# Kernel tuning notes

Measured on AMD Instinct MI355X. Metric: run time of the kernel, lower is better.

The kernel has to match this reference:

```python
import jax, jax.numpy as jnp
import numpy as np

CHANS = [32, 32, 64, 64, 128, 128]
IN_CHANS = [1, 32, 32, 64, 64, 128]
BETA = 0.25  # VectorQuantizer_reset default; ResidualVQ's beta=0.4 is never forwarded
BN_EPS = 1e-5


def setup_inputs() -> dict:
    key = jax.random.key(0)
    ks = jax.random.split(key, 20)
    B, L, IDIM, H, NE = 64, 2000, 80, 256, 1024
    inp = {"speech": jax.random.normal(ks[0], (B, L, IDIM), jnp.float32)}
    for i, (ci, co) in enumerate(zip(IN_CHANS, CHANS)):
        inp[f"cw{i}"] = jax.random.normal(ks[1 + i], (co, ci, 3, 3), jnp.float32) * 0.05
        inp[f"g{i}"] = jnp.ones((co,), jnp.float32)
        inp[f"b{i}"] = jnp.zeros((co,), jnp.float32)
    inp["w_ih"] = jax.random.normal(ks[10], (3 * H, 256), jnp.float32) * 0.05
    inp["w_hh"] = jax.random.normal(ks[11], (3 * H, H), jnp.float32) * 0.05
    inp["bih"] = jnp.zeros((3 * H,), jnp.float32)
    inp["bhh"] = jnp.zeros((3 * H,), jnp.float32)
    for j, k in zip((1, 2, 3), (12, 13, 14)):
        inp[f"cb{j}"] = jax.random.uniform(ks[k], (NE, H), jnp.float32, -1.0 / NE, 1.0 / NE)
    return inp


def conv_bn_relu(x, w, g, b):
    # Conv2d(k=3, stride=2, pad=1, bias=False) + BatchNorm2d (training-mode batch stats) + ReLU
    y = jax.lax.conv_general_dilated(x, w, (2, 2), [(1, 1), (1, 1)],
                                     dimension_numbers=("NCHW", "OIHW", "NCHW"))
    mu = jnp.mean(y, axis=(0, 2, 3), keepdims=True)
    var = jnp.mean((y - mu) ** 2, axis=(0, 2, 3), keepdims=True)  # biased, as torch BN
    y = (y - mu) * jax.lax.rsqrt(var + BN_EPS) * g.reshape(1, -1, 1, 1) + b.reshape(1, -1, 1, 1)
    return jax.nn.relu(y)


def gru_last_hidden(x, w_ih, w_hh, bih, bhh):
    # x: (B, T, D). PyTorch GRU, 1 layer, h0 = 0; returns last hidden state (B, H).
    B = x.shape[0]
    H = w_hh.shape[1]
    xw = jnp.einsum("btd,gd->btg", x, w_ih) + bih  # (B, T, 3H), precompute input gates

    def step(h, xt):
        gh = h @ w_hh.T + bhh
        i_r, i_z, i_n = jnp.split(xt, 3, axis=-1)
        h_r, h_z, h_n = jnp.split(gh, 3, axis=-1)
        r = jax.nn.sigmoid(i_r + h_r)
        z = jax.nn.sigmoid(i_z + h_z)
        n = jnp.tanh(i_n + r * h_n)
        return (1.0 - z) * n + z * h, None

    h0 = jnp.zeros((B, H), x.dtype)
    hT, _ = jax.lax.scan(step, h0, jnp.swapaxes(xw, 0, 1))
    return hT


def vq(z, E):
    # z: (B, e_dim), E: (n_e, e_dim). Nearest-neighbor quantize + straight-through.
    d = jnp.sum(z * z, axis=1, keepdims=True) + jnp.sum(E * E, axis=1) - 2.0 * (z @ E.T)
    idx = jnp.argmin(d, axis=1)  # (B,)
    z_q = E[idx]
    loss = jnp.mean((jax.lax.stop_gradient(z_q) - z) ** 2) \
         + BETA * jnp.mean((z_q - jax.lax.stop_gradient(z)) ** 2)
    z_q_st = z + jax.lax.stop_gradient(z_q - z)
    return z_q_st, loss, idx


def reference(speech, cw0, g0, b0, cw1, g1, b1, cw2, g2, b2, cw3, g3, b3,
              cw4, g4, b4, cw5, g5, b5, w_ih, w_hh, bih, bhh, cb1, cb2, cb3):
    x = speech[:, None, :, :]  # (B, 1, L, idim)
    for w, g, b in ((cw0, g0, b0), (cw1, g1, b1), (cw2, g2, b2),
                    (cw3, g3, b3), (cw4, g4, b4), (cw5, g5, b5)):
        x = conv_bn_relu(x, w, g, b)
    B, C, T, F = x.shape
    hs = x.transpose(0, 2, 1, 3).reshape(B, T, C * F)  # (B, T', C*F)
    ref_embs = gru_last_hidden(hs, w_ih, w_hh, bih, bhh)  # (B, 256)

    residual = ref_embs
    zq1, l1, i1 = vq(residual, cb1)
    residual = residual - zq1
    zq2, l2, i2 = vq(residual, cb2)
    residual = residual - zq2
    zq3, l3, i3 = vq(residual, cb3)

    z_q_out = jnp.concatenate([zq1, zq2, zq3], axis=1)  # (B, 3*e_dim)
    vq_loss = l1 + l2 + l3
    codebooks = (zq1, zq2, zq3, zq1 + zq2 + zq3)
    return (z_q_out, vq_loss, i1[:, None], codebooks)
```

## Files before the change

kernel.cpp:

```cpp
#include <hip/hip_runtime.h>
#include <math.h>


__global__ __launch_bounds__(256) void prep_kernel(
    const float* __restrict__ w_ih, const float* __restrict__ w_hh,
    const float* __restrict__ cb0, const float* __restrict__ cb1,
    const float* __restrict__ cb2, float* __restrict__ w_ihT,
    float* __restrict__ w_hhT, float* __restrict__ ET, float* __restrict__ sE) {
  int tid = threadIdx.x;
  int y = blockIdx.y;
  if (y < 5) {
    const float* in;
    float* outp;
    int R, C;
    if (y == 0) { in = w_ih; outp = w_ihT; R = 768; C = 256; }
    else if (y == 1) { in = w_hh; outp = w_hhT; R = 768; C = 256; }
    else {
      in = (y == 2 ? cb0 : (y == 3 ? cb1 : cb2));
      outp = ET + (size_t)(y - 2) * 262144;
      R = 1024; C = 256;
    }
    int n = R * C;
    for (int t = blockIdx.x * 256 + tid; t < n; t += 64 * 256) {
      int i = t / C, j = t % C;
      outp[(size_t)j * R + i] = in[t];
    }
  } else {
    int wid = tid >> 6, lane = tid & 63;
    for (int c = blockIdx.x * 4 + wid; c < 3072; c += 64 * 4) {
      const float* E = (c < 1024 ? cb0 : (c < 2048 ? cb1 : cb2));
      int cc = c & 1023;
      float4 v4 = ((const float4*)(E + (size_t)cc * 256))[lane];
      float ssum = v4.x * v4.x + v4.y * v4.y + v4.z * v4.z + v4.w * v4.w;
#pragma unroll
      for (int m = 32; m >= 1; m >>= 1) ssum += __shfl_xor(ssum, m, 64);
      if (lane == 0) sE[c] = ssum;
    }
  }
}

__global__ __launch_bounds__(256) void conv0_stats_kernel(
    const float* __restrict__ speech, const float* __restrict__ w0,
    float* __restrict__ part) {
  constexpr int SPR = 41, SPH = 49;
  __shared__ float spE[SPH * SPR];
  __shared__ float spO[SPH * SPR];
  const int tid = threadIdx.x;
  const int bx = blockIdx.x;
  const int b = blockIdx.z;
  const int to0 = bx * 24;
  const int sr0 = 2 * to0 - 1;
  const float* sb = speech + (size_t)b * 160000;
  for (int i = tid; i < SPH * 81; i += 256) {
    int r = i / 81, c = i % 81;
    int gr = sr0 + r, gc = c - 1;
    float v = (gr >= 0 && gr < 2000 && gc >= 0 && gc < 80) ? sb[gr * 80 + gc] : 0.f;
    float* pl = (c & 1) ? spO : spE;
    pl[r * SPR + (c >> 1)] = v;
  }
  __syncthreads();

  const int fo = tid % 40;
  const int trr = tid / 40;
  const bool rowok = (trr < 6);
  const int r0 = rowok ? trr * 4 : 0;

  float xv4[4][9];
  {
    int e0 = (2 * r0) * SPR + fo;
    float p0 = spE[e0], p1 = spO[e0], p2 = spE[e0 + 1];
#pragma unroll
    for (int k = 0; k < 4; ++k) {
      int mr = (2 * (r0 + k) + 1) * SPR + fo;
      int br = mr + SPR;
      xv4[k][0] = p0; xv4[k][1] = p1; xv4[k][2] = p2;
      xv4[k][3] = spE[mr]; xv4[k][4] = spO[mr]; xv4[k][5] = spE[mr + 1];
      xv4[k][6] = spE[br]; xv4[k][7] = spO[br]; xv4[k][8] = spE[br + 1];
      p0 = xv4[k][6]; p1 = xv4[k][7]; p2 = xv4[k][8];
    }
  }
  bool val[4];
#pragma unroll
  for (int k = 0; k < 4; ++k) val[k] = rowok && (to0 + r0 + k < 1000);

  float s[32], q[32];
#pragma unroll
  for (int c = 0; c < 32; ++c) { s[c] = 0.f; q[c] = 0.f; }
#pragma unroll
  for (int c = 0; c < 32; ++c) {
    const float* wk = w0 + c * 9;
    float w0v = wk[0], w1v = wk[1], w2v = wk[2], w3v = wk[3], w4v = wk[4];
    float w5v = wk[5], w6v = wk[6], w7v = wk[7], w8v = wk[8];
#pragma unroll
    for (int k = 0; k < 4; ++k) {
      float a = xv4[k][0] * w0v;
      a = fmaf(xv4[k][1], w1v, a); a = fmaf(xv4[k][2], w2v, a);
      a = fmaf(xv4[k][3], w3v, a); a = fmaf(xv4[k][4], w4v, a);
      a = fmaf(xv4[k][5], w5v, a); a = fmaf(xv4[k][6], w6v, a);
      a = fmaf(xv4[k][7], w7v, a); a = fmaf(xv4[k][8], w8v, a);
      if (val[k]) { s[c] += a; q[c] = fmaf(a, a, q[c]); }
    }
  }
  const int wid = tid >> 6;
  const int lane = tid & 63;
  const int pidx = ((b * 42 + bx) << 2) | wid;
#pragma unroll
  for (int c = 0; c < 32; ++c) {
    float ss = s[c], qq = q[c];
#pragma unroll
    for (int m = 32; m >= 1; m >>= 1) {
      ss += __shfl_xor(ss, m, 64);
      qq += __shfl_xor(qq, m, 64);
    }
    if (lane == 0) {
      part[(size_t)c * 10752 + pidx] = ss;
      part[(size_t)(32 + c) * 10752 + pidx] = qq;
    }
  }
}

__global__ __launch_bounds__(256) void conv1_fused_kernel(
    const float* __restrict__ speech, const float* __restrict__ w0,
    const float* __restrict__ aff0, const float* __restrict__ w1,
    float* __restrict__ y) {
  constexpr int SPR = 41, SPH = 51;
  constexpr int LPS = 21, LTH = 25, LPL = LTH * LPS;
  __shared__ float spE[SPH * SPR];
  __shared__ float spO[SPH * SPR];
  __shared__ float l0t[2][2 * LPL];
  const int tid = threadIdx.x;
  const int bx = blockIdx.x;
  const int b = blockIdx.z;
  const int to0 = bx * 12;
  const int l0r0 = 2 * to0 - 1;
  const int sr0 = 4 * to0 - 3;
  const float* sb = speech + (size_t)b * 160000;
  for (int i = tid; i < SPH * 81; i += 256) {
    int r = i / 81, c = i % 81;
    int gr = sr0 + r, gc = c - 1;
    float v = (gr >= 0 && gr < 2000 && gc >= 0 && gc < 80) ? sb[gr * 80 + gc] : 0.f;
    float* pl = (c & 1) ? spO : spE;
    pl[r * SPR + (c >> 1)] = v;
  }

  const int fc = tid % 42;
  const int fr0 = tid / 42;
  const bool filler = (tid < 210);
  const int wcol = fc - 1;
  const bool colok = (wcol >= 0) && (wcol < 40);
  const int wc = colok ? wcol : 0;
  const int r0 = fr0 * 5;
  const int lplane = (fc & 1) * LPL;
  const int lidx = fc >> 1;

  const int fo = tid % 20;
  const int tr = tid / 20;
  const int to = to0 + tr;
  const bool active = (tr < 12) && (to < 500);
  const int trc = (tr < 12) ? tr : 0;

  float acc[32];
#pragma unroll
  for (int c = 0; c < 32; ++c) acc[c] = 0.f;

  __syncthreads();

#define L0FILL(CIDX, BF)                                                      \
  if (filler) {                                                               \
    const float* wk = w0 + (CIDX) * 9;                                        \
    const float wv0 = wk[0], wv1 = wk[1], wv2 = wk[2], wv3 = wk[3];           \
    const float wv4 = wk[4], wv5 = wk[5], wv6 = wk[6], wv7 = wk[7];           \
    const float wv8 = wk[8];                                                  \
    const float sc = aff0[CIDX], sh = aff0[32 + (CIDX)];                      \
    int e0 = (2 * r0) * SPR + wc;                                             \
    float t0 = spE[e0], t1 = spO[e0], t2 = spE[e0 + 1];                       \
    _Pragma("unroll")                                                         \
    for (int k = 0; k < 5; ++k) {                                             \
      int r = r0 + k;                                                         \
      int mr = (2 * r + 1) * SPR + wc;                                        \
      int br = mr + SPR;                                                      \
      float m0 = spE[mr], m1 = spO[mr], m2 = spE[mr + 1];                     \
      float b0 = spE[br], b1 = spO[br], b2 = spE[br + 1];                     \
      float a = t0 * wv0;                                                     \
      a = fmaf(t1, wv1, a); a = fmaf(t2, wv2, a);                             \
      a = fmaf(m0, wv3, a); a = fmaf(m1, wv4, a); a = fmaf(m2, wv5, a);       \
      a = fmaf(b0, wv6, a); a = fmaf(b1, wv7, a); a = fmaf(b2, wv8, a);       \
      int h0 = l0r0 + r;                                                      \
      bool ok = colok && h0 >= 0 && h0 < 1000;                                \
      float vv = ok ? fmaxf(fmaf(a, sc, sh), 0.f) : 0.f;                      \
      l0t[BF][lplane + r * LPS + lidx] = vv;                                  \
      t0 = b0; t1 = b1; t2 = b2;                                              \
    }                                                                         \
  }

  L0FILL(0, 0)
  __syncthreads();

  for (int ci = 0; ci < 32; ++ci) {
    int cur = ci & 1;
    if (ci + 1 < 32) { L0FILL(ci + 1, cur ^ 1) }
    float xv[9];
    const int rb = 2 * trc;
#pragma unroll
    for (int t = 0; t < 9; ++t) {
      int dr = t / 3, m = t % 3;
      xv[t] = l0t[cur][(m == 1 ? LPL : 0) + (rb + dr) * LPS + fo + (m == 2 ? 1 : 0)];
    }
    const float* wp = w1 + ci * 9;
#pragma unroll
    for (int c = 0; c < 32; ++c) {
      const float* wcp = wp + (size_t)c * 32 * 9;
#pragma unroll
      for (int t = 0; t < 9; ++t) acc[c] = fmaf(xv[t], wcp[t], acc[c]);
    }
    __syncthreads();
  }
#undef L0FILL

  if (active) {
#pragma unroll
    for (int c = 0; c < 32; ++c)
      y[(((size_t)b * 32 + c) * 500 + to) * 20 + fo] = acc[c];
  }
}

template <int CI, int COG, int WO, int ROWS, int WI, int HI, int HO>
__global__ __launch_bounds__(256) void conv_kernel(
    const float* __restrict__ x, const float* __restrict__ w,
    const float* __restrict__ aff, float* __restrict__ y, int CO) {
  constexpr int TW = WI + 2;
  constexpr int PE = (TW + 1) / 2;
  constexpr int PS = PE | 1;
  constexpr int TH = 2 * ROWS + 1;
  constexpr int PL = TH * PS;
  constexpr int TN = TH * TW;
  constexpr int F = (TN + 255) / 256;
  __shared__ float tile[2][2 * PL];

  const int tid = threadIdx.x;
  const int fo = tid % WO;
  const int tr = tid / WO;
  const int to0 = blockIdx.x * ROWS;
  const int to = to0 + tr;
  const int co0 = blockIdx.y * COG;
  const int b = blockIdx.z;
  const bool active = (tr < ROWS) && (to < HO);
  const int trc = (tr < ROWS) ? tr : 0;

  int fa[F], fof[F];
  bool fv[F], fw[F];
#pragma unroll
  for (int j = 0; j < F; ++j) {
    int i = tid + j * 256;
    int r = i / TW, c = i % TW;
    int gih = 2 * to0 - 1 + r;
    int giw = c - 1;
    bool inb = (i < TN);
    bool v = inb && gih >= 0 && gih < HI && giw >= 0 && giw < WI;
    fw[j] = inb;
    fv[j] = v;
    fof[j] = v ? (gih * WI + giw) : 0;
    fa[j] = inb ? ((c & 1) * PL + r * PS + (c >> 1)) : 0;
  }

  float acc[COG];
#pragma unroll
  for (int c = 0; c < COG; ++c) acc[c] = 0.f;

  const float* xb = x + (size_t)b * CI * HI * WI;

  {
    const float sc = aff[0], sh = aff[CI];
#pragma unroll
    for (int j = 0; j < F; ++j) {
      if (fw[j]) {
        float v = xb[fof[j]];
        v = fv[j] ? fmaxf(fmaf(v, sc, sh), 0.f) : 0.f;
        tile[0][fa[j]] = v;
      }
    }
  }
  __syncthreads();

  for (int ci = 0; ci < CI; ++ci) {
    int cur = ci & 1;
    if (ci + 1 < CI) {
      const float* xc = xb + (size_t)(ci + 1) * HI * WI;
      const float sc = aff[ci + 1], sh = aff[CI + ci + 1];
#pragma unroll
      for (int j = 0; j < F; ++j) {
        if (fw[j]) {
          float v = xc[fof[j]];
          v = fv[j] ? fmaxf(fmaf(v, sc, sh), 0.f) : 0.f;
          tile[cur ^ 1][fa[j]] = v;
        }
      }
    }
    float xv[9];
    const int rb = 2 * trc;
#pragma unroll
    for (int t = 0; t < 9; ++t) {
      int dr = t / 3, m = t % 3;
      xv[t] = tile[cur][(m == 1 ? PL : 0) + (rb + dr) * PS + fo + (m == 2 ? 1 : 0)];
    }
    const float* wp = w + ((size_t)co0 * CI + ci) * 9;
#pragma unroll
    for (int c = 0; c < COG; ++c) {
      const float* wc = wp + (size_t)c * CI * 9;
#pragma unroll
      for (int t = 0; t < 9; ++t) acc[c] = fmaf(xv[t], wc[t], acc[c]);
    }
    __syncthreads();
  }

  if (active) {
#pragma unroll
    for (int c = 0; c < COG; ++c)
      y[(((size_t)b * CO + co0 + c) * HO + to) * WO + fo] = acc[c];
  }
}

__global__ __launch_bounds__(256) void conv5_kernel(
    const float* __restrict__ x, const float* __restrict__ w5,
    const float* __restrict__ aff, float* __restrict__ part5) {
  constexpr int TW = 5, PS = 3, TH = 65, PL = TH * PS, TN = TH * TW;
  __shared__ float tile[2][2 * PL];
  const int tid = threadIdx.x;
  const int p = tid & 63;
  const int to = p >> 1, fo = p & 1;
  const int cog = tid >> 6;
  const int co0 = cog * 32;
  const int ci0 = blockIdx.y * 32;
  const int b = blockIdx.z;

  int fa[2], fof[2];
  bool fv[2], fw[2];
#pragma unroll
  for (int j = 0; j < 2; ++j) {
    int i = tid + j * 256;
    int r = i / TW, c = i % TW;
    int gih = r - 1, giw = c - 1;
    bool inb = (i < TN);
    bool v = inb && gih >= 0 && gih < 63 && giw >= 0 && giw < 3;
    fw[j] = inb;
    fv[j] = v;
    fof[j] = v ? (gih * 3 + giw) : 0;
    fa[j] = inb ? ((c & 1) * PL + r * PS + (c >> 1)) : 0;
  }

  float acc[32];
#pragma unroll
  for (int c = 0; c < 32; ++c) acc[c] = 0.f;

  const float* xb = x + (size_t)b * 128 * 189;

  {
    const float sc = aff[ci0], sh = aff[128 + ci0];
    const float* xc = xb + (size_t)ci0 * 189;
#pragma unroll
    for (int j = 0; j < 2; ++j) {
      if (fw[j]) {
        float v = xc[fof[j]];
        v = fv[j] ? fmaxf(fmaf(v, sc, sh), 0.f) : 0.f;
        tile[0][fa[j]] = v;
      }
    }
  }
  __syncthreads();

  for (int cc = 0; cc < 32; ++cc) {
    int cur = cc & 1;
    int ci = ci0 + cc;
    if (cc + 1 < 32) {
      const float* xc = xb + (size_t)(ci + 1) * 189;
      const float sc = aff[ci + 1], sh = aff[128 + ci + 1];
#pragma unroll
      for (int j = 0; j < 2; ++j) {
        if (fw[j]) {
          float v = xc[fof[j]];
          v = fv[j] ? fmaxf(fmaf(v, sc, sh), 0.f) : 0.f;
          tile[cur ^ 1][fa[j]] = v;
        }
      }
    }
    float xv[9];
#pragma unroll
    for (int t = 0; t < 9; ++t) {
      int dr = t / 3, m = t % 3;
      xv[t] = tile[cur][(m == 1 ? PL : 0) + (2 * to + dr) * PS + fo + (m == 2 ? 1 : 0)];
    }
    const float* wp = w5 + ((size_t)co0 * 128 + ci) * 9;
#pragma unroll
    for (int c = 0; c < 32; ++c) {
      const float* wc = wp + (size_t)c * 128 * 9;
#pragma unroll
      for (int t = 0; t < 9; ++t) acc[c] = fmaf(xv[t], wc[t], acc[c]);
    }
    __syncthreads();
  }

#pragma unroll
  for (int c = 0; c < 32; ++c)
    part5[(((size_t)blockIdx.y * 64 + b) * 128 + co0 + c) * 64 + p] = acc[c];
}

__global__ __launch_bounds__(256) void reduce4_kernel(const float* __restrict__ p,
                                                      float* __restrict__ y) {
  int i = blockIdx.x * 256 + threadIdx.x;
  if (i < 524288)
    y[i] = p[i] + p[i + 524288] + p[i + 2 * 524288] + p[i + 3 * 524288];
}

__global__ __launch_bounds__(256) void stats_kernel(const float* __restrict__ x,
                                                    float* __restrict__ part,
                                                    int C, int HW) {
  int c = blockIdx.x, b = blockIdx.y, tid = threadIdx.x;
  const float* xb = x + ((size_t)b * C + c) * HW;
  float s = 0.f, q = 0.f;
  for (int i = tid; i < HW; i += 256) {
    float v = xb[i];
    s += v;
    q = fmaf(v, v, q);
  }
#pragma unroll
  for (int m = 32; m >= 1; m >>= 1) {
    s += __shfl_xor(s, m, 64);
    q += __shfl_xor(q, m, 64);
  }
  if ((tid & 63) == 0) {
    int w = tid >> 6;
    part[(size_t)c * 256 + b * 4 + w] = s;
    part[(size_t)(C + c) * 256 + b * 4 + w] = q;
  }
}

__global__ __launch_bounds__(256) void bn_finalize(
    const float* __restrict__ part, const float* __restrict__ g,
    const float* __restrict__ bb, float* __restrict__ aff, int CO, int P,
    double invN) {
  __shared__ double s1[256];
  __shared__ double s2[256];
  int c = blockIdx.x, tid = threadIdx.x;
  double a = 0, q = 0;
  for (int i = tid; i < P; i += 256) {
    a += (double)part[(size_t)c * P + i];
    q += (double)part[(size_t)(CO + c) * P + i];
  }
  s1[tid] = a;
  s2[tid] = q;
  __syncthreads();
  for (int s = 128; s > 0; s >>= 1) {
    if (tid < s) { s1[tid] += s1[tid + s]; s2[tid] += s2[tid + s]; }
    __syncthreads();
  }
  if (tid == 0) {
    double mean = s1[0] * invN;
    double var = s2[0] * invN - mean * mean;
    float scale = g[c] * (float)(1.0 / sqrt(var + 1e-5));
    aff[c] = scale;
    aff[CO + c] = bb[c] - (float)mean * scale;
  }
}

__global__ __launch_bounds__(256) void xw_kernel(const float* __restrict__ act5,
                                                 const float* __restrict__ aff5,
                                                 const float* __restrict__ w_ihT,
                                                 const float* __restrict__ bih,
                                                 float* __restrict__ xw) {
  __shared__ float sh[8 * 256];
  int tid = threadIdx.x;
  int bt0 = blockIdx.x * 8;
  int b = bt0 >> 5;
  for (int i = tid; i < 2048; i += 256) {
    int r = i >> 8, d = i & 255, c = d >> 1, f = d & 1;
    int t = (bt0 + r) & 31;
    float v = act5[(((size_t)b * 128 + c) * 32 + t) * 2 + f];
    sh[i] = fmaxf(fmaf(v, aff5[c], aff5[128 + c]), 0.f);
  }
  __syncthreads();
  float acc[3][8];
#pragma unroll
  for (int g = 0; g < 3; ++g)
#pragma unroll
    for (int r = 0; r < 8; ++r) acc[g][r] = 0.f;
  for (int k = 0; k < 256; ++k) {
    float w0 = w_ihT[k * 768 + tid];
    float w1 = w_ihT[k * 768 + 256 + tid];
    float w2 = w_ihT[k * 768 + 512 + tid];
#pragma unroll
    for (int r = 0; r < 8; ++r) {
      float hv = sh[r * 256 + k];
      acc[0][r] = fmaf(hv, w0, acc[0][r]);
      acc[1][r] = fmaf(hv, w1, acc[1][r]);
      acc[2][r] = fmaf(hv, w2, acc[2][r]);
    }
  }
  float b0 = bih[tid], b1 = bih[256 + tid], b2 = bih[512 + tid];
  for (int r = 0; r < 8; ++r) {
    size_t base = (size_t)(bt0 + r) * 768;
    xw[base + tid] = acc[0][r] + b0;
    xw[base + 256 + tid] = acc[1][r] + b1;
    xw[base + 512 + tid] = acc[2][r] + b2;
  }
}

__global__ __launch_bounds__(768) void gru_kernel(const float* __restrict__ xw,
                                                  const float* __restrict__ w_hhT,
                                                  const float* __restrict__ bhh,
                                                  float* __restrict__ zout) {
  __shared__ __align__(16) float h[256];
  __shared__ float gh[768];
  int b = blockIdx.x, j = threadIdx.x;
  if (j < 256) h[j] = 0.f;
  __syncthreads();
  float bh = bhh[j];
  for (int t = 0; t < 32; ++t) {
    float acc = 0.f;
    const float4* h4 = (const float4*)h;
#pragma unroll 8
    for (int k4 = 0; k4 < 64; ++k4) {
      float4 hv = h4[k4];
      const float* wr = w_hhT + (4 * k4) * 768 + j;
      acc = fmaf(hv.x, wr[0], acc);
      acc = fmaf(hv.y, wr[768], acc);
      acc = fmaf(hv.z, wr[1536], acc);
      acc = fmaf(hv.w, wr[2304], acc);
    }
    gh[j] = acc + bh;
    __syncthreads();
    if (j < 256) {
      const float* xt = xw + ((size_t)b * 32 + t) * 768;
      float ir = xt[j], iz = xt[256 + j], inn = xt[512 + j];
      float r = 1.f / (1.f + expf(-(ir + gh[j])));
      float zz = 1.f / (1.f + expf(-(iz + gh[256 + j])));
      float n = tanhf(fmaf(r, gh[512 + j], inn));
      h[j] = (1.f - zz) * n + zz * h[j];
    }
    __syncthreads();
  }
  if (j < 256) zout[(size_t)b * 256 + j] = h[j];
}

__global__ __launch_bounds__(256) void vq_all_kernel(
    const float* __restrict__ zb, const float* __restrict__ ET,
    const float* __restrict__ sE, const float* __restrict__ cb0,
    const float* __restrict__ cb1, const float* __restrict__ cb2,
    float* __restrict__ out, float* __restrict__ msep) {
  const size_t OFF_I1 = 49153;
  const size_t OFF_CB = 49217;
  const size_t OFF_CBSUM = 98369;
  __shared__ float rz[256];
  __shared__ float rs[256];
  __shared__ int ri[256];
  int b = blockIdx.x, tid = threadIdx.x;
  float z0 = zb[(size_t)b * 256 + tid];
  rz[tid] = z0;
  float zqs = 0.f;
  for (int s = 0; s < 3; ++s) {
    __syncthreads();
    const float* ETs = ET + (size_t)s * 262144;
    const float* sEs = sE + s * 1024;
    const float* E = (s == 0 ? cb0 : (s == 1 ? cb1 : cb2));
    float a0 = 0.f, a1 = 0.f, a2 = 0.f, a3 = 0.f;
    for (int k = 0; k < 256; ++k) {
      float zk = rz[k];
      const float* row = ETs + (size_t)k * 1024 + tid;
      a0 = fmaf(zk, row[0], a0);
      a1 = fmaf(zk, row[256], a1);
      a2 = fmaf(zk, row[512], a2);
      a3 = fmaf(zk, row[768], a3);
    }
    float s0 = sEs[tid] - 2.f * a0;
    float s1 = sEs[256 + tid] - 2.f * a1;
    float s2 = sEs[512 + tid] - 2.f * a2;
    float s3 = sEs[768 + tid] - 2.f * a3;
    float bs = s0;
    int bi = tid;
    if (s1 < bs) { bs = s1; bi = 256 + tid; }
    if (s2 < bs) { bs = s2; bi = 512 + tid; }
    if (s3 < bs) { bs = s3; bi = 768 + tid; }
    rs[tid] = bs;
    ri[tid] = bi;
    __syncthreads();
    for (int st = 128; st > 0; st >>= 1) {
      if (tid < st) {
        float os = rs[tid + st];
        int oi = ri[tid + st];
        if (os < rs[tid] || (os == rs[tid] && oi < ri[tid])) {
          rs[tid] = os;
          ri[tid] = oi;
        }
      }
      __syncthreads();
    }
    int idx = ri[0];
    if (s == 0 && tid == 0) out[OFF_I1 + b] = (float)idx;
    float zq = E[(size_t)idx * 256 + tid];
    float rv = rz[tid];
    float d = zq - rv;
    out[(size_t)b * 768 + s * 256 + tid] = zq;
    out[OFF_CB + (size_t)s * 16384 + (size_t)b * 256 + tid] = zq;
    zqs += zq;
    rz[tid] = rv - zq;
    rs[tid] = d * d;
    __syncthreads();
    for (int st = 128; st > 0; st >>= 1) {
      if (tid < st) rs[tid] += rs[tid + st];
      __syncthreads();
    }
    if (tid == 0) msep[s * 64 + b] = rs[0];
  }
  out[OFF_CBSUM + (size_t)b * 256 + tid] = zqs;
}

__global__ void loss_kernel(const float* __restrict__ msep, float* __restrict__ out) {
  if (threadIdx.x == 0 && blockIdx.x == 0) {
    float s = 0.f;
    for (int i = 0; i < 192; ++i) s += msep[i];
    out[0] = 1.25f * s / 16384.0f;
  }
}

extern "C" void kernel_launch(void* const* d_in, const int* in_sizes, int n_in,
                              void* d_out, int out_size, void* d_ws, size_t ws_size,
                              hipStream_t stream) {
  const float* speech = (const float*)d_in[0];
  const float* cw[6];
  const float* gg[6];
  const float* bbp[6];
  for (int i = 0; i < 6; ++i) {
    cw[i] = (const float*)d_in[1 + 3 * i];
    gg[i] = (const float*)d_in[2 + 3 * i];
    bbp[i] = (const float*)d_in[3 + 3 * i];
  }
  const float* w_ih = (const float*)d_in[19];
  const float* w_hh = (const float*)d_in[20];
  const float* bih = (const float*)d_in[21];
  const float* bhh = (const float*)d_in[22];
  const float* cb[3] = {(const float*)d_in[23], (const float*)d_in[24], (const float*)d_in[25]};
  float* out = (float*)d_out;
  float* ws_f = (float*)d_ws;
  (void)in_sizes; (void)n_in; (void)out_size;

  size_t off = 0;
  float* act1 = ws_f + off; off += 20480000ull;
  float* act2 = ws_f + off; off += 10240000ull;
  float* act3 = ws_f + off; off += 2560000ull;
  float* part = ws_f + off; off += 700000ull;
  float* affs = ws_f + off; off += 1536ull;
  float* w_ihT = ws_f + off; off += 196608ull;
  float* w_hhT = ws_f + off; off += 196608ull;
  float* xw = ws_f + off; off += 1572864ull;
  float* zb = ws_f + off; off += 16384ull;
  float* ET = ws_f + off; off += 786432ull;
  float* sEp = ws_f + off; off += 3072ull;
  float* msep = ws_f + off; off += 192ull;

  if (ws_size < off * sizeof(float)) return;

  float* part5 = act1;
  float* act4 = act2;
  float* act5 = act3;

  const size_t OFF_LOSS = 49152;

  prep_kernel<<<dim3(64, 6), 256, 0, stream>>>(w_ih, w_hh, cb[0], cb[1], cb[2],
                                               w_ihT, w_hhT, ET, sEp);

  conv0_stats_kernel<<<dim3(42, 1, 64), 256, 0, stream>>>(speech, cw[0], part);
  bn_finalize<<<32, 256, 0, stream>>>(part, gg[0], bbp[0], affs + 0, 32, 10752,
                                      1.0 / 2560000.0);
  conv1_fused_kernel<<<dim3(42, 1, 64), 256, 0, stream>>>(speech, cw[0], affs + 0,
                                                          cw[1], act1);
  stats_kernel<<<dim3(32, 64), 256, 0, stream>>>(act1, part, 32, 10000);
  bn_finalize<<<32, 256, 0, stream>>>(part, gg[1], bbp[1], affs + 256, 32, 256,
                                      1.0 / 640000.0);
  conv_kernel<32, 32, 10, 25, 20, 500, 250>
      <<<dim3(10, 2, 64), 256, 0, stream>>>(act1, cw[2], affs + 256, act2, 64);
  stats_kernel<<<dim3(64, 64), 256, 0, stream>>>(act2, part, 64, 2500);
  bn_finalize<<<64, 256, 0, stream>>>(part, gg[2], bbp[2], affs + 512, 64, 256,
                                      1.0 / 160000.0);
  conv_kernel<64, 16, 5, 42, 10, 250, 125>
      <<<dim3(3, 4, 64), 256, 0, stream>>>(act2, cw[3], affs + 512, act3, 64);
  stats_kernel<<<dim3(64, 64), 256, 0, stream>>>(act3, part, 64, 625);
  bn_finalize<<<64, 256, 0, stream>>>(part, gg[3], bbp[3], affs + 768, 64, 256,
                                      1.0 / 40000.0);
  conv_kernel<64, 16, 3, 63, 5, 125, 63>
      <<<dim3(1, 8, 64), 256, 0, stream>>>(act3, cw[4], affs + 768, act4, 128);
  stats_kernel<<<dim3(128, 64), 256, 0, stream>>>(act4, part, 128, 189);
  bn_finalize<<<128, 256, 0, stream>>>(part, gg[4], bbp[4], affs + 1024, 128, 256,
                                       1.0 / 12096.0);
  conv5_kernel<<<dim3(1, 4, 64), 256, 0, stream>>>(act4, cw[5], affs + 1024, part5);
  reduce4_kernel<<<2048, 256, 0, stream>>>(part5, act5);
  stats_kernel<<<dim3(128, 64), 256, 0, stream>>>(act5, part, 128, 64);
  bn_finalize<<<128, 256, 0, stream>>>(part, gg[5], bbp[5], affs + 1280, 128, 256,
                                       1.0 / 4096.0);

  xw_kernel<<<256, 256, 0, stream>>>(act5, affs + 1280, w_ihT, bih, xw);
  gru_kernel<<<64, 768, 0, stream>>>(xw, w_hhT, bhh, zb);

  vq_all_kernel<<<64, 256, 0, stream>>>(zb, ET, sEp, cb[0], cb[1], cb[2], out, msep);
  loss_kernel<<<1, 64, 0, stream>>>(msep, out + OFF_LOSS);
}
```

Baseline: 1.182 ms.

## Recompute layer-0 conv in registers inside conv1, drop shared staging and barriers

Replaces the conv1 kernel that staged BN-ReLU'd layer-0 outputs per input channel in double-buffered shared memory with a kernel where each thread loads a 7x7 input patch into registers and recomputes its 3x3 layer-0 neighbourhood per channel. This removes per-channel __syncthreads and shared traffic, and uses a 240-thread block so all threads produce outputs. A pre-transposed copy of the conv1 weights is produced in the prep kernel for contiguous per-channel access. The cost is redundant layer-0 FMAs across neighbouring threads and higher register pressure.

After: 1.210 ms. 2.3% more time.

```diff
diff --git a/kernel.cpp b/kernel.cpp
--- a/kernel.cpp
+++ b/kernel.cpp
@@ -5,8 +5,9 @@
 __global__ __launch_bounds__(256) void prep_kernel(
     const float* __restrict__ w_ih, const float* __restrict__ w_hh,
     const float* __restrict__ cb0, const float* __restrict__ cb1,
-    const float* __restrict__ cb2, float* __restrict__ w_ihT,
-    float* __restrict__ w_hhT, float* __restrict__ ET, float* __restrict__ sE) {
+    const float* __restrict__ cb2, const float* __restrict__ cw1,
+    float* __restrict__ w_ihT, float* __restrict__ w_hhT,
+    float* __restrict__ ET, float* __restrict__ sE, float* __restrict__ w1T) {
   int tid = threadIdx.x;
   int y = blockIdx.y;
   if (y < 5) {
@@ -25,7 +26,7 @@
       int i = t / C, j = t % C;
       outp[(size_t)j * R + i] = in[t];
     }
-  } else {
+  } else if (y == 5) {
     int wid = tid >> 6, lane = tid & 63;
     for (int c = blockIdx.x * 4 + wid; c < 3072; c += 64 * 4) {
       const float* E = (c < 1024 ? cb0 : (c < 2048 ? cb1 : cb2));
@@ -35,6 +36,14 @@
 #pragma unroll
       for (int m = 32; m >= 1; m >>= 1) ssum += __shfl_xor(ssum, m, 64);
       if (lane == 0) sE[c] = ssum;
+    }
+  } else {
+    for (int t = blockIdx.x * 256 + tid; t < 9216; t += 64 * 256) {
+      int q = t % 9;
+      int rc = t / 9;
+      int co = rc % 32;
+      int ci = rc / 32;
+      w1T[t] = cw1[((size_t)co * 32 + ci) * 9 + q];
     }
   }
 }
@@ -119,105 +128,77 @@
   }
 }
 
-__global__ __launch_bounds__(256) void conv1_fused_kernel(
+__global__ __launch_bounds__(240) void conv1_reg_kernel(
     const float* __restrict__ speech, const float* __restrict__ w0,
-    const float* __restrict__ aff0, const float* __restrict__ w1,
+    const float* __restrict__ aff0, const float* __restrict__ w1T,
     float* __restrict__ y) {
-  constexpr int SPR = 41, SPH = 51;
-  constexpr int LPS = 21, LTH = 25, LPL = LTH * LPS;
-  __shared__ float spE[SPH * SPR];
-  __shared__ float spO[SPH * SPR];
-  __shared__ float l0t[2][2 * LPL];
+  __shared__ float sp[51 * 84];
   const int tid = threadIdx.x;
   const int bx = blockIdx.x;
   const int b = blockIdx.z;
   const int to0 = bx * 12;
-  const int l0r0 = 2 * to0 - 1;
   const int sr0 = 4 * to0 - 3;
   const float* sb = speech + (size_t)b * 160000;
-  for (int i = tid; i < SPH * 81; i += 256) {
-    int r = i / 81, c = i % 81;
-    int gr = sr0 + r, gc = c - 1;
-    float v = (gr >= 0 && gr < 2000 && gc >= 0 && gc < 80) ? sb[gr * 80 + gc] : 0.f;
-    float* pl = (c & 1) ? spO : spE;
-    pl[r * SPR + (c >> 1)] = v;
-  }
-
-  const int fc = tid % 42;
-  const int fr0 = tid / 42;
-  const bool filler = (tid < 210);
-  const int wcol = fc - 1;
-  const bool colok = (wcol >= 0) && (wcol < 40);
-  const int wc = colok ? wcol : 0;
-  const int r0 = fr0 * 5;
-  const int lplane = (fc & 1) * LPL;
-  const int lidx = fc >> 1;
+  for (int i = tid; i < 51 * 84; i += 240) {
+    int r = i / 84, c = i % 84;
+    int gr = sr0 + r, gc = c - 3;
+    sp[i] = (gr >= 0 && gr < 2000 && gc >= 0 && gc < 80) ? sb[gr * 80 + gc] : 0.f;
+  }
+  __syncthreads();
 
   const int fo = tid % 20;
   const int tr = tid / 20;
   const int to = to0 + tr;
-  const bool active = (tr < 12) && (to < 500);
-  const int trc = (tr < 12) ? tr : 0;
+
+  float s[49];
+  {
+    const float* base = sp + (4 * tr) * 84 + 4 * fo;
+#pragma unroll
+    for (int i = 0; i < 7; ++i)
+#pragma unroll
+      for (int j = 0; j < 7; ++j) s[i * 7 + j] = base[i * 84 + j];
+  }
+
+  bool rv[3], cv[3];
+#pragma unroll
+  for (int d = 0; d < 3; ++d) {
+    int h0 = 2 * to - 1 + d;
+    rv[d] = (h0 >= 0 && h0 < 1000);
+    int wq = 2 * fo - 1 + d;
+    cv[d] = (wq >= 0 && wq < 40);
+  }
 
   float acc[32];
 #pragma unroll
   for (int c = 0; c < 32; ++c) acc[c] = 0.f;
 
-  __syncthreads();
-
-#define L0FILL(CIDX, BF)                                                      \
-  if (filler) {                                                               \
-    const float* wk = w0 + (CIDX) * 9;                                        \
-    const float wv0 = wk[0], wv1 = wk[1], wv2 = wk[2], wv3 = wk[3];           \
-    const float wv4 = wk[4], wv5 = wk[5], wv6 = wk[6], wv7 = wk[7];           \
-    const float wv8 = wk[8];                                                  \
-    const float sc = aff0[CIDX], sh = aff0[32 + (CIDX)];                      \
-    int e0 = (2 * r0) * SPR + wc;                                             \
-    float t0 = spE[e0], t1 = spO[e0], t2 = spE[e0 + 1];                       \
-    _Pragma("unroll")                                                         \
-    for (int k = 0; k < 5; ++k) {                                             \
-      int r = r0 + k;                                                         \
-      int mr = (2 * r + 1) * SPR + wc;                                        \
-      int br = mr + SPR;                                                      \
-      float m0 = spE[mr], m1 = spO[mr], m2 = spE[mr + 1];                     \
-      float b0 = spE[br], b1 = spO[br], b2 = spE[br + 1];                     \
-      float a = t0 * wv0;                                                     \
-      a = fmaf(t1, wv1, a); a = fmaf(t2, wv2, a);                             \
-      a = fmaf(m0, wv3, a); a = fmaf(m1, wv4, a); a = fmaf(m2, wv5, a);       \
-      a = fmaf(b0, wv6, a); a = fmaf(b1, wv7, a); a = fmaf(b2, wv8, a);       \
-      int h0 = l0r0 + r;                                                      \
-      bool ok = colok && h0 >= 0 && h0 < 1000;                                \
-      float vv = ok ? fmaxf(fmaf(a, sc, sh), 0.f) : 0.f;                      \
-      l0t[BF][lplane + r * LPS + lidx] = vv;                                  \
-      t0 = b0; t1 = b1; t2 = b2;                                              \
-    }                                                                         \
-  }
-
-  L0FILL(0, 0)
-  __syncthreads();
-
   for (int ci = 0; ci < 32; ++ci) {
-    int cur = ci & 1;
-    if (ci + 1 < 32) { L0FILL(ci + 1, cur ^ 1) }
-    float xv[9];
-    const int rb = 2 * trc;
-#pragma unroll
-    for (int t = 0; t < 9; ++t) {
-      int dr = t / 3, m = t % 3;
-      xv[t] = l0t[cur][(m == 1 ? LPL : 0) + (rb + dr) * LPS + fo + (m == 2 ? 1 : 0)];
-    }
-    const float* wp = w1 + ci * 9;
+    const float* wk = w0 + ci * 9;
+    const float sc = aff0[ci], sh = aff0[32 + ci];
+    float l0v[9];
+#pragma unroll
+    for (int dr = 0; dr < 3; ++dr) {
+#pragma unroll
+      for (int dc = 0; dc < 3; ++dc) {
+        float a = 0.f;
+#pragma unroll
+        for (int kr = 0; kr < 3; ++kr)
+#pragma unroll
+          for (int kc = 0; kc < 3; ++kc)
+            a = fmaf(s[(2 * dr + kr) * 7 + 2 * dc + kc], wk[kr * 3 + kc], a);
+        float v = fmaxf(fmaf(a, sc, sh), 0.f);
+        l0v[dr * 3 + dc] = (rv[dr] && cv[dc]) ? v : 0.f;
+      }
+    }
+    const float* wp = w1T + ci * 288;
 #pragma unroll
     for (int c = 0; c < 32; ++c) {
-      const float* wcp = wp + (size_t)c * 32 * 9;
-#pragma unroll
-      for (int t = 0; t < 9; ++t) acc[c] = fmaf(xv[t], wcp[t], acc[c]);
-    }
-    __syncthreads();
-  }
-#undef L0FILL
-
-  if (active) {
+#pragma unroll
+      for (int q = 0; q < 9; ++q) acc[c] = fmaf(l0v[q], wp[c * 9 + q], acc[c]);
+    }
+  }
+
+  if (to < 500) {
 #pragma unroll
     for (int c = 0; c < 32; ++c)
       y[(((size_t)b * 32 + c) * 500 + to) * 20 + fo] = acc[c];
@@ -655,6 +636,7 @@
   float* ET = ws_f + off; off += 786432ull;
   float* sEp = ws_f + off; off += 3072ull;
   float* msep = ws_f + off; off += 192ull;
+  float* w1T = ws_f + off; off += 9216ull;
 
   if (ws_size < off * sizeof(float)) return;
 
@@ -664,14 +646,14 @@
 
   const size_t OFF_LOSS = 49152;
 
-  prep_kernel<<<dim3(64, 6), 256, 0, stream>>>(w_ih, w_hh, cb[0], cb[1], cb[2],
-                                               w_ihT, w_hhT, ET, sEp);
+  prep_kernel<<<dim3(64, 7), 256, 0, stream>>>(w_ih, w_hh, cb[0], cb[1], cb[2],
+                                               cw[1], w_ihT, w_hhT, ET, sEp, w1T);
 
   conv0_stats_kernel<<<dim3(42, 1, 64), 256, 0, stream>>>(speech, cw[0], part);
   bn_finalize<<<32, 256, 0, stream>>>(part, gg[0], bbp[0], affs + 0, 32, 10752,
                                       1.0 / 2560000.0);
-  conv1_fused_kernel<<<dim3(42, 1, 64), 256, 0, stream>>>(speech, cw[0], affs + 0,
-                                                          cw[1], act1);
+  conv1_reg_kernel<<<dim3(42, 1, 64), 240, 0, stream>>>(speech, cw[0], affs + 0,
+                                                        w1T, act1);
   stats_kernel<<<dim3(32, 64), 256, 0, stream>>>(act1, part, 32, 10000);
   bn_finalize<<<32, 256, 0, stream>>>(part, gg[1], bbp[1], affs + 256, 32, 256,
                                       1.0 / 640000.0);
```

## Fuse BatchNorm statistics into conv epilogues and drop separate stats kernels

Applied to the files above, without the earlier changes.

Each conv kernel now computes per-wavefront partial sums and sums of squares of its outputs in registers and writes them to the partials buffer. The separate stats_kernel launches, which reread every activation tensor, are removed. The final reduce of conv5 partials also emits the stats. bn_finalize now reduces over more partials per channel, and the stats are taken from fp32 accumulators in a different summation order.

New measurement: 1.199 ms. Within noise of the previous version (+1.4%).

```diff
diff --git a/kernel.cpp b/kernel.cpp
--- a/kernel.cpp
+++ b/kernel.cpp
@@ -122,7 +122,7 @@
 __global__ __launch_bounds__(256) void conv1_fused_kernel(
     const float* __restrict__ speech, const float* __restrict__ w0,
     const float* __restrict__ aff0, const float* __restrict__ w1,
-    float* __restrict__ y) {
+    float* __restrict__ y, float* __restrict__ part) {
   constexpr int SPR = 41, SPH = 51;
   constexpr int LPS = 21, LTH = 25, LPL = LTH * LPS;
   __shared__ float spE[SPH * SPR];
@@ -222,12 +222,31 @@
     for (int c = 0; c < 32; ++c)
       y[(((size_t)b * 32 + c) * 500 + to) * 20 + fo] = acc[c];
   }
+
+  const int wid = tid >> 6;
+  const int lane = tid & 63;
+  const int pidx = ((b * 42 + bx) << 2) | wid;
+#pragma unroll
+  for (int c = 0; c < 32; ++c) {
+    float v = active ? acc[c] : 0.f;
+    float qq = v * v;
+#pragma unroll
+    for (int m = 32; m >= 1; m >>= 1) {
+      v += __shfl_xor(v, m, 64);
+      qq += __shfl_xor(qq, m, 64);
+    }
+    if (lane == 0) {
+      part[(size_t)c * 10752 + pidx] = v;
+      part[(size_t)(32 + c) * 10752 + pidx] = qq;
+    }
+  }
 }
 
 template <int CI, int COG, int WO, int ROWS, int WI, int HI, int HO>
 __global__ __launch_bounds__(256) void conv_kernel(
     const float* __restrict__ x, const float* __restrict__ w,
-    const float* __restrict__ aff, float* __restrict__ y, int CO) {
+    const float* __restrict__ aff, float* __restrict__ y, int CO,
+    float* __restrict__ part) {
   constexpr int TW = WI + 2;
   constexpr int PE = (TW + 1) / 2;
   constexpr int PS = PE | 1;
@@ -317,6 +336,25 @@
 #pragma unroll
     for (int c = 0; c < COG; ++c)
       y[(((size_t)b * CO + co0 + c) * HO + to) * WO + fo] = acc[c];
+  }
+
+  const int wid = tid >> 6;
+  const int lane = tid & 63;
+  const int P = (int)(gridDim.z * gridDim.x) * 4;
+  const int pidx = ((b * (int)gridDim.x + (int)blockIdx.x) << 2) | wid;
+#pragma unroll
+  for (int c = 0; c < COG; ++c) {
+    float v = active ? acc[c] : 0.f;
+    float qq = v * v;
+#pragma unroll
+    for (int m = 32; m >= 1; m >>= 1) {
+      v += __shfl_xor(v, m, 64);
+      qq += __shfl_xor(qq, m, 64);
+    }
+    if (lane == 0) {
+      part[(size_t)(co0 + c) * P + pidx] = v;
+      part[(size_t)(CO + co0 + c) * P + pidx] = qq;
+    }
   }
 }
 
@@ -404,33 +442,24 @@
     part5[(((size_t)blockIdx.y * 64 + b) * 128 + co0 + c) * 64 + p] = acc[c];
 }
 
-__global__ __launch_bounds__(256) void reduce4_kernel(const float* __restrict__ p,
-                                                      float* __restrict__ y) {
+__global__ __launch_bounds__(256) void reduce4st_kernel(const float* __restrict__ p,
+                                                        float* __restrict__ y,
+                                                        float* __restrict__ part) {
   int i = blockIdx.x * 256 + threadIdx.x;
-  if (i < 524288)
-    y[i] = p[i] + p[i + 524288] + p[i + 2 * 524288] + p[i + 3 * 524288];
-}
-
-__global__ __launch_bounds__(256) void stats_kernel(const float* __restrict__ x,
-                                                    float* __restrict__ part,
-                                                    int C, int HW) {
-  int c = blockIdx.x, b = blockIdx.y, tid = threadIdx.x;
-  const float* xb = x + ((size_t)b * C + c) * HW;
-  float s = 0.f, q = 0.f;
-  for (int i = tid; i < HW; i += 256) {
-    float v = xb[i];
-    s += v;
-    q = fmaf(v, v, q);
-  }
+  float s = p[i] + p[i + 524288] + p[i + 2 * 524288] + p[i + 3 * 524288];
+  y[i] = s;
+  float q = s * s;
+  float ss = s;
 #pragma unroll
   for (int m = 32; m >= 1; m >>= 1) {
-    s += __shfl_xor(s, m, 64);
+    ss += __shfl_xor(ss, m, 64);
     q += __shfl_xor(q, m, 64);
   }
-  if ((tid & 63) == 0) {
-    int w = tid >> 6;
-    part[(size_t)c * 256 + b * 4 + w] = s;
-    part[(size_t)(C + c) * 256 + b * 4 + w] = q;
+  if ((threadIdx.x & 63) == 0) {
+    int c = (i >> 6) & 127;
+    int b = i >> 13;
+    part[(size_t)c * 64 + b] = ss;
+    part[(size_t)(128 + c) * 64 + b] = q;
   }
 }
 
@@ -671,29 +700,24 @@
   bn_finalize<<<32, 256, 0, stream>>>(part, gg[0], bbp[0], affs + 0, 32, 10752,
                                       1.0 / 2560000.0);
   conv1_fused_kernel<<<dim3(42, 1, 64), 256, 0, stream>>>(speech, cw[0], affs + 0,
-                                                          cw[1], act1);
-  stats_kernel<<<dim3(32, 64), 256, 0, stream>>>(act1, part, 32, 10000);
-  bn_finalize<<<32, 256, 0, stream>>>(part, gg[1], bbp[1], affs + 256, 32, 256,
+                                                          cw[1], act1, part);
+  bn_finalize<<<32, 256, 0, stream>>>(part, gg[1], bbp[1], affs + 256, 32, 10752,
                                       1.0 / 640000.0);
   conv_kernel<32, 32, 10, 25, 20, 500, 250>
-      <<<dim3(10, 2, 64), 256, 0, stream>>>(act1, cw[2], affs + 256, act2, 64);
-  stats_kernel<<<dim3(64, 64), 256, 0, stream>>>(act2, part, 64, 2500);
-  bn_finalize<<<64, 256, 0, stream>>>(part, gg[2], bbp[2], affs + 512, 64, 256,
+      <<<dim3(10, 2, 64), 256, 0, stream>>>(act1, cw[2], affs + 256, act2, 64, part);
+  bn_finalize<<<64, 256, 0, stream>>>(part, gg[2], bbp[2], affs + 512, 64, 2560,
                                       1.0 / 160000.0);
   conv_kernel<64, 16, 5, 42, 10, 250, 125>
-      <<<dim3(3, 4, 64), 256, 0, stream>>>(act2, cw[3], affs + 512, act3, 64);
-  stats_kernel<<<dim3(64, 64), 256, 0, stream>>>(act3, part, 64, 625);
-  bn_finalize<<<64, 256, 0, stream>>>(part, gg[3], bbp[3], affs + 768, 64, 256,
+      <<<dim3(3, 4, 64), 256, 0, stream>>>(act2, cw[3], affs + 512, act3, 64, part);
+  bn_finalize<<<64, 256, 0, stream>>>(part, gg[3], bbp[3], affs + 768, 64, 768,
                                       1.0 / 40000.0);
   conv_kernel<64, 16, 3, 63, 5, 125, 63>
-      <<<dim3(1, 8, 64), 256, 0, stream>>>(act3, cw[4], affs + 768, act4, 128);
-  stats_kernel<<<dim3(128, 64), 256, 0, stream>>>(act4, part, 128, 189);
+      <<<dim3(1, 8, 64), 256, 0, stream>>>(act3, cw[4], affs + 768, act4, 128, part);
   bn_finalize<<<128, 256, 0, stream>>>(part, gg[4], bbp[4], affs + 1024, 128, 256,
                                        1.0 / 12096.0);
   conv5_kernel<<<dim3(1, 4, 64), 256, 0, stream>>>(act4, cw[5], affs + 1024, part5);
-  reduce4_kernel<<<2048, 256, 0, stream>>>(part5, act5);
-  stats_kernel<<<dim3(128, 64), 256, 0, stream>>>(act5, part, 128, 64);
-  bn_finalize<<<128, 256, 0, stream>>>(part, gg[5], bbp[5], affs + 1280, 128, 256,
+  reduce4st_kernel<<<2048, 256, 0, stream>>>(part5, act5, part);
+  bn_finalize<<<128, 256, 0, stream>>>(part, gg[5], bbp[5], affs + 1280, 128, 64,
                                        1.0 / 4096.0);
 
   xw_kernel<<<256, 256, 0, stream>>>(act5, affs + 1280, w_ihT, bih, xw);
```
